# Kernel optimization log

Measured on AMD Instinct MI355X. Metric: run time of the kernel, lower is better.

The kernel has to match this reference:

```python
import jax, jax.numpy as jnp
import numpy as np

IN_F = 4096
OUT_F = 4096
RANK = 8
ALPHA = 8
SCALE = ALPHA / RANK


def setup_inputs() -> dict:
    key = jax.random.key(0)
    kx, kw, kb, ka = jax.random.split(key, 4)
    x = jax.random.normal(kx, (4, 4096, IN_F), dtype=jnp.float32)
    # base frozen linear params (torch Linear default init style, any values ok)
    W = jax.random.normal(kw, (OUT_F, IN_F), dtype=jnp.float32) * (1.0 / np.sqrt(IN_F))
    b = jax.random.normal(kb, (OUT_F,), dtype=jnp.float32) * 0.01
    # lora_A: kaiming_uniform_(a=sqrt(5)) -> U(-bound, bound), bound = sqrt(6/((1+5)*in_f)) = 1/sqrt(in_f)
    bound = 1.0 / np.sqrt(IN_F)
    lora_A = jax.random.uniform(ka, (RANK, IN_F), dtype=jnp.float32, minval=-bound, maxval=bound)
    # lora_B initialized to zeros per module; use small random values so the LoRA path is exercised
    lora_B = jax.random.normal(jax.random.fold_in(key, 7), (OUT_F, RANK), dtype=jnp.float32) * 0.02
    return {"x": x, "W": W, "b": b, "lora_A": lora_A, "lora_B": lora_B}


def reference(x, W, b, lora_A, lora_B):
    # base: x @ W.T + b  [B,S,out_f]
    base = jnp.einsum("bsi,oi->bso", x, W) + b
    # low-rank path: (x @ A.T) @ B.T * scale
    xa = jnp.einsum("bsi,ri->bsr", x, lora_A)  # [B,S,r]
    lora = jnp.einsum("bsr,or->bso", xa, lora_B)
    return base + lora * SCALE
```

## Files before the change

### kernel.cpp

```cpp
#include <hip/hip_runtime.h>
#include <cstdint>

#define K_IN   4096
#define N_OUT  4096
#define M_ROWS 16384
#define RANK   8
#define LSCALE 1.0f
#define NT     64
#define ROWB   8192
#define AHALF  1048576

typedef __attribute__((ext_vector_type(8))) short  short8;
typedef __attribute__((ext_vector_type(4))) float  floatx4;

__device__ __forceinline__ unsigned short f2bf(float f) {
  uint32_t u = __float_as_uint(f);
  u += 0x7FFFu + ((u >> 16) & 1u);
  return (unsigned short)(u >> 16);
}

__global__ __launch_bounds__(256) void fold_w_kernel(
    const float* __restrict__ W, const float* __restrict__ lA,
    const float* __restrict__ lB, unsigned short* __restrict__ Weff) {
  int idx = blockIdx.x * 256 + threadIdx.x;
  int o = idx >> 10;
  int k = (idx & 1023) << 2;
  float4 w = *reinterpret_cast<const float4*>(W + (size_t)o * K_IN + k);
#pragma unroll
  for (int r = 0; r < RANK; ++r) {
    float s = LSCALE * lB[o * RANK + r];
    float4 a = *reinterpret_cast<const float4*>(lA + r * K_IN + k);
    w.x += s * a.x; w.y += s * a.y; w.z += s * a.z; w.w += s * a.w;
  }
  ushort4 p;
  p.x = f2bf(w.x); p.y = f2bf(w.y); p.z = f2bf(w.z); p.w = f2bf(w.w);
  *reinterpret_cast<ushort4*>(Weff + (size_t)o * K_IN + k) = p;
}

__global__ __launch_bounds__(256) void cvt_x_kernel(
    const float* __restrict__ x, unsigned short* __restrict__ xb) {
  size_t i = ((size_t)blockIdx.x * 256 + threadIdx.x) * 8;
  float4 a = *reinterpret_cast<const float4*>(x + i);
  float4 c = *reinterpret_cast<const float4*>(x + i + 4);
  uint4 v;
  v.x = (uint32_t)f2bf(a.x) | ((uint32_t)f2bf(a.y) << 16);
  v.y = (uint32_t)f2bf(a.z) | ((uint32_t)f2bf(a.w) << 16);
  v.z = (uint32_t)f2bf(c.x) | ((uint32_t)f2bf(c.y) << 16);
  v.w = (uint32_t)f2bf(c.z) | ((uint32_t)f2bf(c.w) << 16);
  *reinterpret_cast<uint4*>(xb + i) = v;
}

__device__ __forceinline__ void gload_lds16(const void* g, void* l) {
  __builtin_amdgcn_global_load_lds(
      (const __attribute__((address_space(1))) void*)g,
      (__attribute__((address_space(3))) void*)l, 16, 0, 0);
}

#define BAR() do { asm volatile("" ::: "memory");                         \
    __builtin_amdgcn_s_barrier();                                         \
    asm volatile("" ::: "memory"); } while (0)

#define DSR(DST, ADDR, IMM)                                               \
  asm volatile("ds_read_b128 %0, %1 offset:%2"                            \
               : "=v"(DST) : "v"(ADDR), "i"(IMM))
#define LGKM(N) do {                                                      \
    asm volatile("s_waitcnt lgkmcnt(" #N ")" ::: "memory");               \
    __builtin_amdgcn_sched_barrier(0); } while (0)

__global__ __launch_bounds__(512, 2) void gemm256_kernel(
    const unsigned short* __restrict__ Xb, const unsigned short* __restrict__ Wb,
    const float* __restrict__ bias, float* __restrict__ out) {
  __shared__ alignas(16) char lds[2 * 65536];

  const int tid  = threadIdx.x;
  const int wave = tid >> 6, lane = tid & 63;
  const int wr = wave >> 2, wc = wave & 3;
  const int l15 = lane & 15, sq = lane >> 4;

  int bx  = blockIdx.x;
  int sbx = (bx & 7) * 128 + (bx >> 3);
  const int mt = sbx >> 4;
  const int nt = sbx & 15;

  const int rstg = tid >> 3;
  const int cbst = (((tid & 7) ^ ((tid >> 3) & 7)) << 4);
  const char* aBase = (const char*)Xb + (size_t)(mt * 256 + rstg) * ROWB + cbst;
  const char* bBase = (const char*)Wb + (size_t)(nt * 256 + rstg) * ROWB + cbst;

#define STAGE_TH(TH, HH) do {                                             \
    const char* src_ = ((HH) < 2 ? aBase + (size_t)(HH) * AHALF           \
                                 : bBase + (size_t)((HH) - 2) * AHALF)    \
                       + (TH) * 128;                                      \
    char* dst_ = lds + ((TH) & 1) * 65536 + (HH) * 16384 + tid * 16;      \
    gload_lds16(src_, dst_);                                              \
    gload_lds16(src_ + (size_t)64 * ROWB, dst_ + 8192);                   \
  } while (0)

  const unsigned ldsb = (unsigned)(unsigned long long)
      (__attribute__((address_space(3))) char*)lds;
  const unsigned X = (unsigned)((l15 & 7) << 4);
  const unsigned aRow = ldsb + wr * 16384 + l15 * 128;
  const unsigned bRow = ldsb + (2 + (wc >> 1)) * 16384 + (wc & 1) * 8192
                        + l15 * 128;
  unsigned aCur0 = aRow + ((0u  + sq * 16) ^ X);
  unsigned aCur1 = aRow + ((64u + sq * 16) ^ X);
  unsigned bCur0 = bRow + ((0u  + sq * 16) ^ X);
  unsigned bCur1 = bRow + ((64u + sq * 16) ^ X);

#define LOAD_A(DST, MQ) do {                                              \
    _Pragma("unroll")                                                     \
    for (int fi = 0; fi < 4; ++fi)                                        \
      DSR(DST[fi],     aCur0, (MQ) * 8192 + fi * 2048);                   \
    _Pragma("unroll")                                                     \
    for (int fi = 0; fi < 4; ++fi)                                        \
      DSR(DST[4 + fi], aCur1, (MQ) * 8192 + fi * 2048);                   \
  } while (0)
#define LOAD_B(DST, NQ) do {                                              \
    _Pragma("unroll")                                                     \
    for (int fj = 0; fj < 2; ++fj)                                        \
      DSR(DST[fj],     bCur0, (NQ) * 4096 + fj * 2048);                   \
    _Pragma("unroll")                                                     \
    for (int fj = 0; fj < 2; ++fj)                                        \
      DSR(DST[2 + fj], bCur1, (NQ) * 4096 + fj * 2048);                   \
  } while (0)
#define MFMA_Q(MQ, NQ, AF, BF) do {                                       \
    __builtin_amdgcn_s_setprio(1);                                        \
    _Pragma("unroll")                                                     \
    for (int ks = 0; ks < 2; ++ks)                                        \
      _Pragma("unroll")                                                   \
      for (int fi = 0; fi < 4; ++fi)                                      \
        _Pragma("unroll")                                                 \
        for (int fj = 0; fj < 2; ++fj)                                    \
          acc[(MQ) * 4 + fi][(NQ) * 2 + fj] =                             \
              __builtin_amdgcn_mfma_f32_16x16x32_bf16(                    \
                  AF[ks * 4 + fi], BF[ks * 2 + fj],                       \
                  acc[(MQ) * 4 + fi][(NQ) * 2 + fj], 0, 0, 0);            \
    __builtin_amdgcn_s_setprio(0); } while (0)

  floatx4 acc[8][4];
#pragma unroll
  for (int i = 0; i < 8; ++i)
#pragma unroll
    for (int j = 0; j < 4; ++j)
      acc[i][j] = (floatx4){0.f, 0.f, 0.f, 0.f};

  STAGE_TH(0, 0); STAGE_TH(0, 1); STAGE_TH(0, 2); STAGE_TH(0, 3);
  STAGE_TH(1, 0); STAGE_TH(1, 1); STAGE_TH(1, 2);
  asm volatile("s_waitcnt vmcnt(6)" ::: "memory");
  BAR();

  short8 afA[8], afB[8], bfC[4], bfD[4];
  LOAD_A(afA, 0);
  LOAD_B(bfC, 0);

  for (int t = 0; t < NT; ++t) {
    LOAD_B(bfD, 1);
    LOAD_A(afB, 1);
    if (t <= NT - 2) STAGE_TH(t + 1, 3);
    LGKM(12);
    MFMA_Q(0, 0, afA, bfC);
    BAR();

    LGKM(8);
    MFMA_Q(0, 1, afA, bfD);
    BAR();

    LGKM(0);
    MFMA_Q(1, 0, afB, bfC);
    if (t <= NT - 2) asm volatile("s_waitcnt vmcnt(0)" ::: "memory");
    BAR();

    if (t <= NT - 2) {
      aCur0 ^= 65536u; aCur1 ^= 65536u; bCur0 ^= 65536u; bCur1 ^= 65536u;
      LOAD_A(afA, 0);
      LOAD_B(bfC, 0);
    }
    if (t <= NT - 3) {
      STAGE_TH(t + 2, 0); STAGE_TH(t + 2, 1); STAGE_TH(t + 2, 2);
    }
    __builtin_amdgcn_sched_barrier(0);
    MFMA_Q(1, 1, afB, bfD);
    BAR();
  }
#undef STAGE_TH
#undef LOAD_A
#undef LOAD_B
#undef MFMA_Q

  const int row0 = mt * 256 + wr * 128 + sq * 4;
  const int col0 = nt * 256 + wc * 64 + l15;
#pragma unroll
  for (int j = 0; j < 4; ++j) {
    int col = col0 + j * 16;
    float bv = bias[col];
#pragma unroll
    for (int i = 0; i < 8; ++i) {
      int rowb = row0 + i * 16;
#pragma unroll
      for (int rr = 0; rr < 4; ++rr)
        out[(size_t)(rowb + rr) * N_OUT + col] = acc[i][j][rr] + bv;
    }
  }
}

__global__ __launch_bounds__(256) void fallback_kernel(
    const float* __restrict__ x, const float* __restrict__ W,
    const float* __restrict__ bias, const float* __restrict__ lA,
    const float* __restrict__ lB, float* __restrict__ out) {
  __shared__ float Xs[64][17];
  __shared__ float Ws[64][17];
  int tid = threadIdx.x;
  int tx = tid & 15, ty = tid >> 4;
  int bm = blockIdx.y * 64, bn = blockIdx.x * 64;
  float acc[4][4] = {};
  for (int k0 = 0; k0 < K_IN; k0 += 16) {
#pragma unroll
    for (int q = 0; q < 4; ++q) {
      int flat = q * 256 + tid;
      int r = flat >> 4, c = flat & 15;
      Xs[r][c] = x[(size_t)(bm + r) * K_IN + k0 + c];
      float w = W[(size_t)(bn + r) * K_IN + k0 + c];
#pragma unroll
      for (int rr = 0; rr < RANK; ++rr)
        w += LSCALE * lB[(bn + r) * RANK + rr] * lA[rr * K_IN + k0 + c];
      Ws[r][c] = w;
    }
    __syncthreads();
#pragma unroll
    for (int kk = 0; kk < 16; ++kk) {
      float av[4], bv[4];
#pragma unroll
      for (int i = 0; i < 4; ++i) av[i] = Xs[ty * 4 + i][kk];
#pragma unroll
      for (int j = 0; j < 4; ++j) bv[j] = Ws[tx * 4 + j][kk];
#pragma unroll
      for (int i = 0; i < 4; ++i)
#pragma unroll
        for (int j = 0; j < 4; ++j) acc[i][j] += av[i] * bv[j];
    }
    __syncthreads();
  }
#pragma unroll
  for (int i = 0; i < 4; ++i)
#pragma unroll
    for (int j = 0; j < 4; ++j)
      out[(size_t)(bm + ty * 4 + i) * N_OUT + bn + tx * 4 + j] =
          acc[i][j] + bias[bn + tx * 4 + j];
}

extern "C" void kernel_launch(void* const* d_in, const int* in_sizes, int n_in,
                              void* d_out, int out_size, void* d_ws, size_t ws_size,
                              hipStream_t stream) {
  const float* x  = (const float*)d_in[0];
  const float* W  = (const float*)d_in[1];
  const float* b  = (const float*)d_in[2];
  const float* lA = (const float*)d_in[3];
  const float* lB = (const float*)d_in[4];
  float* out = (float*)d_out;

  const size_t weff_bytes = (size_t)N_OUT * K_IN * 2;
  const size_t xb_bytes   = (size_t)M_ROWS * K_IN * 2;

  if (ws_size >= weff_bytes + xb_bytes) {
    unsigned short* Weff = (unsigned short*)d_ws;
    unsigned short* Xb   = (unsigned short*)((char*)d_ws + weff_bytes);
    fold_w_kernel<<<(int)(((size_t)N_OUT * K_IN / 4) / 256), 256, 0, stream>>>(W, lA, lB, Weff);
    cvt_x_kernel<<<(int)(((size_t)M_ROWS * K_IN / 8) / 256), 256, 0, stream>>>(x, Xb);
    gemm256_kernel<<<(M_ROWS / 256) * (N_OUT / 256), 512, 0, stream>>>(Xb, Weff, b, out);
  } else {
    dim3 grid(N_OUT / 64, M_ROWS / 64);
    fallback_kernel<<<grid, 256, 0, stream>>>(x, W, b, lA, lB, out);
  }
}
```

Baseline: 583.6 us.

## Restructure GEMM main loop LDS read and global staging schedule

Reworks the software pipeline of the bf16 MFMA GEMM loop. All four quarter-tiles of the next-next k-tile are now staged together after the third MFMA quarter, rather than the last quarter being issued at the top of the iteration. The LDS fragment reads are split into smaller groups interleaved between MFMA quarters, with tighter lgkmcnt waits. The intent is to hide LDS read latency behind MFMA work and simplify the vmcnt bookkeeping. The trade-off is that global loads are issued in larger bursts, and the unconditional vmcnt(0) wait inside each iteration may stall the loop.

```diff
diff --git a/kernel.cpp b/kernel.cpp
--- a/kernel.cpp
+++ b/kernel.cpp
@@ -95,6 +95,9 @@
     gload_lds16(src_, dst_);                                              \
     gload_lds16(src_ + (size_t)64 * ROWB, dst_ + 8192);                   \
   } while (0)
+#define STAGE_TILE(TH) do {                                               \
+    STAGE_TH(TH, 0); STAGE_TH(TH, 1); STAGE_TH(TH, 2); STAGE_TH(TH, 3);   \
+  } while (0)
 
   const unsigned ldsb = (unsigned)(unsigned long long)
       (__attribute__((address_space(3))) char*)lds;
@@ -107,21 +110,11 @@
   unsigned bCur0 = bRow + ((0u  + sq * 16) ^ X);
   unsigned bCur1 = bRow + ((64u + sq * 16) ^ X);
 
-#define LOAD_A(DST, MQ) do {                                              \
-    _Pragma("unroll")                                                     \
-    for (int fi = 0; fi < 4; ++fi)                                        \
-      DSR(DST[fi],     aCur0, (MQ) * 8192 + fi * 2048);                   \
-    _Pragma("unroll")                                                     \
-    for (int fi = 0; fi < 4; ++fi)                                        \
-      DSR(DST[4 + fi], aCur1, (MQ) * 8192 + fi * 2048);                   \
-  } while (0)
-#define LOAD_B(DST, NQ) do {                                              \
-    _Pragma("unroll")                                                     \
-    for (int fj = 0; fj < 2; ++fj)                                        \
-      DSR(DST[fj],     bCur0, (NQ) * 4096 + fj * 2048);                   \
-    _Pragma("unroll")                                                     \
-    for (int fj = 0; fj < 2; ++fj)                                        \
-      DSR(DST[2 + fj], bCur1, (NQ) * 4096 + fj * 2048);                   \
+#define LOAD_B4(DST, NQ) do {                                             \
+    DSR(DST[0], bCur0, (NQ) * 4096);                                      \
+    DSR(DST[1], bCur0, (NQ) * 4096 + 2048);                               \
+    DSR(DST[2], bCur1, (NQ) * 4096);                                      \
+    DSR(DST[3], bCur1, (NQ) * 4096 + 2048);                               \
   } while (0)
 #define MFMA_Q(MQ, NQ, AF, BF) do {                                       \
     __builtin_amdgcn_s_setprio(1);                                        \
@@ -144,47 +137,63 @@
     for (int j = 0; j < 4; ++j)
       acc[i][j] = (floatx4){0.f, 0.f, 0.f, 0.f};
 
-  STAGE_TH(0, 0); STAGE_TH(0, 1); STAGE_TH(0, 2); STAGE_TH(0, 3);
-  STAGE_TH(1, 0); STAGE_TH(1, 1); STAGE_TH(1, 2);
-  asm volatile("s_waitcnt vmcnt(6)" ::: "memory");
+  STAGE_TILE(0);
+  STAGE_TILE(1);
+  asm volatile("s_waitcnt vmcnt(8)" ::: "memory");
   BAR();
 
   short8 afA[8], afB[8], bfC[4], bfD[4];
-  LOAD_A(afA, 0);
-  LOAD_B(bfC, 0);
+#pragma unroll
+  for (int fi = 0; fi < 4; ++fi) DSR(afA[fi],     aCur0, fi * 2048);
+#pragma unroll
+  for (int fi = 0; fi < 4; ++fi) DSR(afA[4 + fi], aCur1, fi * 2048);
+  LOAD_B4(bfC, 0);
 
   for (int t = 0; t < NT; ++t) {
-    LOAD_B(bfD, 1);
-    LOAD_A(afB, 1);
-    if (t <= NT - 2) STAGE_TH(t + 1, 3);
-    LGKM(12);
+    LOAD_B4(bfD, 1);
+    DSR(afB[0], aCur0, 8192);
+    DSR(afB[1], aCur0, 8192 + 2048);
+    LGKM(6);
     MFMA_Q(0, 0, afA, bfC);
     BAR();
 
+    DSR(afB[2], aCur0, 8192 + 2 * 2048);
+    DSR(afB[3], aCur0, 8192 + 3 * 2048);
+    DSR(afB[4], aCur1, 8192);
+    DSR(afB[5], aCur1, 8192 + 2048);
+    DSR(afB[6], aCur1, 8192 + 2 * 2048);
+    DSR(afB[7], aCur1, 8192 + 3 * 2048);
     LGKM(8);
     MFMA_Q(0, 1, afA, bfD);
-    BAR();
-
-    LGKM(0);
-    MFMA_Q(1, 0, afB, bfC);
-    if (t <= NT - 2) asm volatile("s_waitcnt vmcnt(0)" ::: "memory");
+    asm volatile("s_waitcnt vmcnt(0)" ::: "memory");
     BAR();
 
     if (t <= NT - 2) {
       aCur0 ^= 65536u; aCur1 ^= 65536u; bCur0 ^= 65536u; bCur1 ^= 65536u;
-      LOAD_A(afA, 0);
-      LOAD_B(bfC, 0);
-    }
-    if (t <= NT - 3) {
-      STAGE_TH(t + 2, 0); STAGE_TH(t + 2, 1); STAGE_TH(t + 2, 2);
-    }
+#pragma unroll
+      for (int fi = 0; fi < 4; ++fi) DSR(afA[fi], aCur0, fi * 2048);
+      DSR(afA[4], aCur1, 0);
+      DSR(afA[5], aCur1, 2048);
+      LGKM(6);
+    } else {
+      LGKM(0);
+    }
+    MFMA_Q(1, 0, afB, bfC);
+    BAR();
+
+    if (t <= NT - 2) {
+      DSR(afA[6], aCur1, 2 * 2048);
+      DSR(afA[7], aCur1, 3 * 2048);
+      LOAD_B4(bfC, 0);
+    }
+    if (t <= NT - 3) STAGE_TILE(t + 2);
     __builtin_amdgcn_sched_barrier(0);
     MFMA_Q(1, 1, afB, bfD);
     BAR();
   }
 #undef STAGE_TH
-#undef LOAD_A
-#undef LOAD_B
+#undef STAGE_TILE
+#undef LOAD_B4
 #undef MFMA_Q
 
   const int row0 = mt * 256 + wr * 128 + sq * 4;
```

Measured after the change: 649.7 us. 1.11x slower.

## Load W fragments directly from global into registers, bypassing LDS

Applied to the files above, without the earlier changes.

B-operand (weight) fragments are now fetched with per-lane global_load_dwordx4 straight into registers instead of being staged through LDS. This halves the LDS footprint, and the pipeline changes from a 1.75-tile lookahead to a single-tile prefetch of A. The tile order is swapped so consecutive blocks share an N-tile, which favours cache reuse of W. The intent is to cut LDS traffic and capacity pressure. The costs are uncoalesced-ish global loads of B that are duplicated across the two wave rows, plus shorter prefetch distance and exposed global latency in the MFMA loop.

```diff
diff --git a/kernel.cpp b/kernel.cpp
--- a/kernel.cpp
+++ b/kernel.cpp
@@ -66,11 +66,17 @@
 #define LGKM(N) do {                                                      \
     asm volatile("s_waitcnt lgkmcnt(" #N ")" ::: "memory");               \
     __builtin_amdgcn_sched_barrier(0); } while (0)
+#define VMW(N) do {                                                       \
+    asm volatile("s_waitcnt vmcnt(" #N ")" ::: "memory");                 \
+    __builtin_amdgcn_sched_barrier(0); } while (0)
+#define GLB(DST, VOFF, IMM)                                               \
+  asm volatile("global_load_dwordx4 %0, %1, %2 offset:%3"                 \
+               : "=v"(DST) : "v"(VOFF), "s"(Wb), "i"(IMM))
 
 __global__ __launch_bounds__(512, 2) void gemm256_kernel(
     const unsigned short* __restrict__ Xb, const unsigned short* __restrict__ Wb,
     const float* __restrict__ bias, float* __restrict__ out) {
-  __shared__ alignas(16) char lds[2 * 65536];
+  __shared__ alignas(16) char lds[2 * 32768];
 
   const int tid  = threadIdx.x;
   const int wave = tid >> 6, lane = tid & 63;
@@ -79,33 +85,34 @@
 
   int bx  = blockIdx.x;
   int sbx = (bx & 7) * 128 + (bx >> 3);
-  const int mt = sbx >> 4;
-  const int nt = sbx & 15;
+  const int nt = sbx >> 6;
+  const int mt = sbx & 63;
 
   const int rstg = tid >> 3;
   const int cbst = (((tid & 7) ^ ((tid >> 3) & 7)) << 4);
   const char* aBase = (const char*)Xb + (size_t)(mt * 256 + rstg) * ROWB + cbst;
-  const char* bBase = (const char*)Wb + (size_t)(nt * 256 + rstg) * ROWB + cbst;
-
-#define STAGE_TH(TH, HH) do {                                             \
-    const char* src_ = ((HH) < 2 ? aBase + (size_t)(HH) * AHALF           \
-                                 : bBase + (size_t)((HH) - 2) * AHALF)    \
-                       + (TH) * 128;                                      \
-    char* dst_ = lds + ((TH) & 1) * 65536 + (HH) * 16384 + tid * 16;      \
-    gload_lds16(src_, dst_);                                              \
-    gload_lds16(src_ + (size_t)64 * ROWB, dst_ + 8192);                   \
+
+#define STAGE_A(TH) do {                                                  \
+    const char* s0_ = aBase + (TH) * 128;                                 \
+    char* d0_ = lds + ((TH) & 1) * 32768 + tid * 16;                      \
+    gload_lds16(s0_, d0_);                                                \
+    gload_lds16(s0_ + (size_t)64 * ROWB, d0_ + 8192);                     \
+    const char* s1_ = s0_ + AHALF;                                        \
+    gload_lds16(s1_, d0_ + 16384);                                        \
+    gload_lds16(s1_ + (size_t)64 * ROWB, d0_ + 24576);                    \
   } while (0)
 
   const unsigned ldsb = (unsigned)(unsigned long long)
       (__attribute__((address_space(3))) char*)lds;
   const unsigned X = (unsigned)((l15 & 7) << 4);
   const unsigned aRow = ldsb + wr * 16384 + l15 * 128;
-  const unsigned bRow = ldsb + (2 + (wc >> 1)) * 16384 + (wc & 1) * 8192
-                        + l15 * 128;
   unsigned aCur0 = aRow + ((0u  + sq * 16) ^ X);
   unsigned aCur1 = aRow + ((64u + sq * 16) ^ X);
-  unsigned bCur0 = bRow + ((0u  + sq * 16) ^ X);
-  unsigned bCur1 = bRow + ((64u + sq * 16) ^ X);
+
+  unsigned vb00 = (unsigned)(nt * 256 + wc * 64 + l15) * ROWB + sq * 16;
+  unsigned vb01 = vb00 + 16u * ROWB;
+  unsigned vb10 = vb00 + 32u * ROWB;
+  unsigned vb11 = vb00 + 48u * ROWB;
 
 #define LOAD_A(DST, MQ) do {                                              \
     _Pragma("unroll")                                                     \
@@ -115,14 +122,10 @@
     for (int fi = 0; fi < 4; ++fi)                                        \
       DSR(DST[4 + fi], aCur1, (MQ) * 8192 + fi * 2048);                   \
   } while (0)
-#define LOAD_B(DST, NQ) do {                                              \
-    _Pragma("unroll")                                                     \
-    for (int fj = 0; fj < 2; ++fj)                                        \
-      DSR(DST[fj],     bCur0, (NQ) * 4096 + fj * 2048);                   \
-    _Pragma("unroll")                                                     \
-    for (int fj = 0; fj < 2; ++fj)                                        \
-      DSR(DST[2 + fj], bCur1, (NQ) * 4096 + fj * 2048);                   \
-  } while (0)
+#define LOAD_BC() do { GLB(bfC[0], vb00, 0); GLB(bfC[1], vb01, 0);        \
+    GLB(bfC[2], vb00, 64); GLB(bfC[3], vb01, 64); } while (0)
+#define LOAD_BD() do { GLB(bfD[0], vb10, 0); GLB(bfD[1], vb11, 0);        \
+    GLB(bfD[2], vb10, 64); GLB(bfD[3], vb11, 64); } while (0)
 #define MFMA_Q(MQ, NQ, AF, BF) do {                                       \
     __builtin_amdgcn_s_setprio(1);                                        \
     _Pragma("unroll")                                                     \
@@ -144,47 +147,48 @@
     for (int j = 0; j < 4; ++j)
       acc[i][j] = (floatx4){0.f, 0.f, 0.f, 0.f};
 
-  STAGE_TH(0, 0); STAGE_TH(0, 1); STAGE_TH(0, 2); STAGE_TH(0, 3);
-  STAGE_TH(1, 0); STAGE_TH(1, 1); STAGE_TH(1, 2);
-  asm volatile("s_waitcnt vmcnt(6)" ::: "memory");
+  short8 afA[8], afB[8], bfC[4], bfD[4];
+
+  STAGE_A(0);
+  LOAD_BC();
+  LOAD_BD();
+  VMW(8);
   BAR();
-
-  short8 afA[8], afB[8], bfC[4], bfD[4];
   LOAD_A(afA, 0);
-  LOAD_B(bfC, 0);
 
   for (int t = 0; t < NT; ++t) {
-    LOAD_B(bfD, 1);
     LOAD_A(afB, 1);
-    if (t <= NT - 2) STAGE_TH(t + 1, 3);
-    LGKM(12);
+    if (t <= NT - 2) { STAGE_A(t + 1); }
+    LGKM(8);
+    if (t <= NT - 2) VMW(8); else VMW(4);
     MFMA_Q(0, 0, afA, bfC);
     BAR();
 
-    LGKM(8);
+    if (t <= NT - 2) VMW(4); else VMW(0);
     MFMA_Q(0, 1, afA, bfD);
     BAR();
 
     LGKM(0);
     MFMA_Q(1, 0, afB, bfC);
-    if (t <= NT - 2) asm volatile("s_waitcnt vmcnt(0)" ::: "memory");
-    BAR();
-
     if (t <= NT - 2) {
-      aCur0 ^= 65536u; aCur1 ^= 65536u; bCur0 ^= 65536u; bCur1 ^= 65536u;
+      vb00 += 128; vb01 += 128; vb10 += 128; vb11 += 128;
+      LOAD_BC();
+      VMW(4);
+    }
+    BAR();
+
+    if (t <= NT - 2) {
+      aCur0 ^= 32768u; aCur1 ^= 32768u;
       LOAD_A(afA, 0);
-      LOAD_B(bfC, 0);
-    }
-    if (t <= NT - 3) {
-      STAGE_TH(t + 2, 0); STAGE_TH(t + 2, 1); STAGE_TH(t + 2, 2);
-    }
-    __builtin_amdgcn_sched_barrier(0);
+    }
     MFMA_Q(1, 1, afB, bfD);
-    BAR();
-  }
-#undef STAGE_TH
+    if (t <= NT - 2) LOAD_BD();
+    BAR();
+  }
+#undef STAGE_A
 #undef LOAD_A
-#undef LOAD_B
+#undef LOAD_BC
+#undef LOAD_BD
 #undef MFMA_Q
 
   const int row0 = mt * 256 + wr * 128 + sq * 4;
```

Result: slower. 807.2 us (+38.3%).
